# Optimization experiments

Measured on AMD Instinct MI355X. Metric: run time of the kernel, lower is better.

The kernel has to match this reference:

```python
import jax, jax.numpy as jnp
import numpy as np

EPS = 0.07      # sinkhorn temperature
ITERS = 7       # sinkhorn iterations
TINY = 1e-8
NORM_EPS = 1e-12  # F.normalize default clamp


def setup_inputs() -> dict:
    key = jax.random.key(0)
    k1, k2 = jax.random.split(key)
    x = jax.random.normal(k1, (64, 2048, 24, 12), dtype=jnp.float32)
    anchors = jax.random.normal(k2, (2, 2048), dtype=jnp.float32) * 0.02
    return {"x": x, "anchors": anchors}


def reference(x, anchors):
    B, C, H, W = x.shape
    HW = H * W
    # tokens: (B, HW, C)
    X = x.reshape(B, C, HW).transpose(0, 2, 1)
    Xn = X / jnp.maximum(jnp.linalg.norm(X, axis=-1, keepdims=True), NORM_EPS)
    An = anchors / jnp.maximum(jnp.linalg.norm(anchors, axis=-1, keepdims=True), NORM_EPS)
    # cosine cost (B, HW, 2)
    Cmat = 1.0 - jnp.einsum('bhc,kc->bhk', Xn, An)
    Kmat = jnp.exp(-Cmat / max(EPS, TINY)) + TINY
    a = jnp.full((B, HW), 1.0 / HW, dtype=Kmat.dtype)
    b = jnp.full((B, 2), 0.5, dtype=Kmat.dtype)

    def step(carry, _):
        u, v = carry
        Kv = jnp.einsum('bhk,bk->bh', Kmat, v) + TINY
        u = a / Kv
        KTu = jnp.einsum('bhk,bh->bk', Kmat, u) + TINY
        v = b / KTu
        return (u, v), None

    u0 = jnp.ones((B, HW), dtype=Kmat.dtype)
    v0 = jnp.ones((B, 2), dtype=Kmat.dtype)
    (u, v), _ = jax.lax.scan(step, (u0, v0), None, length=ITERS)
    # transport plan and soft masks
    P = Kmat * u[:, :, None] * v[:, None, :]          # (B, HW, 2)
    m = (P * HW).transpose(0, 2, 1).reshape(B, 2, H, W)
    # masked pooling for both prototypes at once
    num = jnp.einsum('bchw,bkhw->bkc', x, m)           # (B, 2, C)
    den = m.sum(axis=(2, 3)) + 1e-6                    # (B, 2)
    c = num / den[:, :, None]
    c0_vec = c[:, 0][:, :, None, None]                 # (B, C, 1, 1)
    c1_vec = c[:, 1][:, :, None, None]
    return (c0_vec, c1_vec, m)
```

## Files before the change

kernel.cpp:

```cpp
#include <hip/hip_runtime.h>

#define B_    64
#define C_    2048
#define HW_   288
#define EPS_  0.07f
#define TINY_ 1e-8f

__device__ __forceinline__ void acc3(const float4 v, float a0, float a1,
                                     float* ssq, float* sd0, float* sd1) {
  ssq[0] += v.x * v.x; ssq[1] += v.y * v.y; ssq[2] += v.z * v.z; ssq[3] += v.w * v.w;
  sd0[0] += v.x * a0;  sd0[1] += v.y * a0;  sd0[2] += v.z * a0;  sd0[3] += v.w * a0;
  sd1[0] += v.x * a1;  sd1[1] += v.y * a1;  sd1[2] += v.z * a1;  sd1[3] += v.w * a1;
}

__global__ __launch_bounds__(256) void k1_partials(
    const float* __restrict__ x, const float* __restrict__ anchors,
    float* __restrict__ part, int nch, int cpc) {
  int bi = blockIdx.x;
  int nblk = nch >> 2;
  int b  = bi / nblk;
  int cg = bi - b * nblk;
  int t = threadIdx.x, lane = t & 63, wid = t >> 6;
  int ch = cg * 4 + wid;
  int c0 = ch * cpc;
  const float* xb = x + ((size_t)b * C_ + c0) * HW_;
  bool tail = lane < 8;

  float ssq[4] = {0,0,0,0}, sd0[4] = {0,0,0,0}, sd1[4] = {0,0,0,0};
  float tsq[4] = {0,0,0,0}, td0[4] = {0,0,0,0}, td1[4] = {0,0,0,0};

#pragma unroll 4
  for (int r = 0; r < cpc; ++r) {
    const float4* xr = (const float4*)(xb + (size_t)r * HW_);
    float a0 = anchors[c0 + r];
    float a1 = anchors[C_ + c0 + r];
    float4 xa = xr[lane];
    acc3(xa, a0, a1, ssq, sd0, sd1);
    if (tail) {
      float4 xc = xr[64 + lane];
      acc3(xc, a0, a1, tsq, td0, td1);
    }
  }

  size_t PS = (size_t)B_ * nch * HW_;
  float* base = part + (size_t)(b * nch + ch) * HW_;
  float4* p0 = (float4*)base;
  float4* p1 = (float4*)(base + PS);
  float4* p2 = (float4*)(base + 2 * PS);
  p0[lane] = make_float4(ssq[0], ssq[1], ssq[2], ssq[3]);
  p1[lane] = make_float4(sd0[0], sd0[1], sd0[2], sd0[3]);
  p2[lane] = make_float4(sd1[0], sd1[1], sd1[2], sd1[3]);
  if (tail) {
    p0[64 + lane] = make_float4(tsq[0], tsq[1], tsq[2], tsq[3]);
    p1[64 + lane] = make_float4(td0[0], td0[1], td0[2], td0[3]);
    p2[64 + lane] = make_float4(td1[0], td1[1], td1[2], td1[3]);
  }
}

__global__ __launch_bounds__(256) void k1b_reduce(
    const float* __restrict__ part, float* __restrict__ red, int nch) {
  int idx = blockIdx.x * 256 + threadIdx.x;
  int plane = idx / (B_ * HW_);
  int rem = idx - plane * (B_ * HW_);
  int b = rem / HW_;
  int h = rem - b * HW_;
  const float* p = part + (size_t)plane * B_ * nch * HW_ + (size_t)b * nch * HW_ + h;
  float s = 0.f;
#pragma unroll 8
  for (int ch = 0; ch < nch; ++ch) s += p[(size_t)ch * HW_];
  red[idx] = s;
}

__device__ __forceinline__ void block_reduce2(
    float& p0, float& p1, volatile float* red0, volatile float* red1,
    int t, int nw) {
  int lane = t & 63, wid = t >> 6;
#pragma unroll
  for (int off = 32; off >= 1; off >>= 1) {
    p0 += __shfl_down(p0, off);
    p1 += __shfl_down(p1, off);
  }
  __syncthreads();
  if (lane == 0) { red0[wid] = p0; red1[wid] = p1; }
  __syncthreads();
  float s0 = 0.f, s1 = 0.f;
  for (int w = 0; w < nw; ++w) { s0 += red0[w]; s1 += red1[w]; }
  p0 = s0; p1 = s1;
}

__global__ __launch_bounds__(320) void k2_sinkhorn(
    const float* __restrict__ red, const float* __restrict__ anchors,
    float* __restrict__ out_m, float* __restrict__ invden) {
  int b = blockIdx.x, t = threadIdx.x;
  __shared__ float red0[8], red1[8];
  const int nw = 5;

  float a0 = 0.f, a1 = 0.f;
  for (int c = t; c < C_; c += 320) {
    float q0 = anchors[c], q1 = anchors[C_ + c];
    a0 += q0 * q0; a1 += q1 * q1;
  }
  block_reduce2(a0, a1, red0, red1, t, nw);
  float ian0 = 1.0f / fmaxf(sqrtf(a0), 1e-12f);
  float ian1 = 1.0f / fmaxf(sqrtf(a1), 1e-12f);

  float K0 = 0.f, K1 = 0.f;
  if (t < HW_) {
    float ssq = red[b * HW_ + t];
    float d0  = red[B_ * HW_ + b * HW_ + t];
    float d1  = red[2 * B_ * HW_ + b * HW_ + t];
    float ixn = 1.0f / fmaxf(sqrtf(ssq), 1e-12f);
    float cos0 = d0 * ixn * ian0;
    float cos1 = d1 * ixn * ian1;
    K0 = expf((cos0 - 1.0f) / EPS_) + TINY_;
    K1 = expf((cos1 - 1.0f) / EPS_) + TINY_;
  }

  float v0 = 1.f, v1 = 1.f, u = 0.f;
  for (int it = 0; it < 7; ++it) {
    if (t < HW_) u = (1.0f / (float)HW_) / (K0 * v0 + K1 * v1 + TINY_);
    float p0 = K0 * u, p1 = K1 * u;
    block_reduce2(p0, p1, red0, red1, t, nw);
    v0 = 0.5f / (p0 + TINY_);
    v1 = 0.5f / (p1 + TINY_);
  }

  float m0 = 0.f, m1 = 0.f;
  if (t < HW_) {
    m0 = K0 * u * v0 * (float)HW_;
    m1 = K1 * u * v1 * (float)HW_;
  }
  float q0 = m0, q1 = m1;
  block_reduce2(q0, q1, red0, red1, t, nw);
  if (t < HW_) {
    out_m[(b * 2 + 0) * HW_ + t] = m0;
    out_m[(b * 2 + 1) * HW_ + t] = m1;
  }
  if (t == 0) {
    invden[b * 2 + 0] = 1.0f / (q0 + 1e-6f);
    invden[b * 2 + 1] = 1.0f / (q1 + 1e-6f);
  }
}

__global__ __launch_bounds__(256) void k3_pool(
    const float* __restrict__ x, const float* __restrict__ m,
    const float* __restrict__ invden, float* __restrict__ out) {
  int bi = blockIdx.x;
  int b = bi >> 3, seg = bi & 7;
  int t = threadIdx.x, oct = t & 7, rl = t >> 3;

  const float4* m0 = (const float4*)(m + (b * 2 + 0) * HW_);
  const float4* m1 = (const float4*)(m + (b * 2 + 1) * HW_);
  float4 w0[9], w1[9];
#pragma unroll
  for (int j = 0; j < 9; ++j) {
    w0[j] = m0[oct * 9 + j];
    w1[j] = m1[oct * 9 + j];
  }
  float inv0 = invden[2 * b], inv1 = invden[2 * b + 1];

  int cbase = seg * 256;
#pragma unroll 2
  for (int g = 0; g < 8; ++g) {
    int c = cbase + g * 32 + rl;
    const float4* xr = (const float4*)(x + ((size_t)b * C_ + c) * HW_) + oct * 9;
    float a0 = 0.f, a1 = 0.f;
#pragma unroll
    for (int j = 0; j < 9; ++j) {
      float4 xa = xr[j];
      a0 += xa.x * w0[j].x + xa.y * w0[j].y + xa.z * w0[j].z + xa.w * w0[j].w;
      a1 += xa.x * w1[j].x + xa.y * w1[j].y + xa.z * w1[j].z + xa.w * w1[j].w;
    }
#pragma unroll
    for (int off = 4; off >= 1; off >>= 1) {
      a0 += __shfl_xor(a0, off);
      a1 += __shfl_xor(a1, off);
    }
    if (oct == 0) {
      out[(size_t)b * C_ + c] = a0 * inv0;
      out[(size_t)B_ * C_ + (size_t)b * C_ + c] = a1 * inv1;
    }
  }
}

extern "C" void kernel_launch(void* const* d_in, const int* in_sizes, int n_in,
                              void* d_out, int out_size, void* d_ws, size_t ws_size,
                              hipStream_t stream) {
  const float* x       = (const float*)d_in[0];
  const float* anchors = (const float*)d_in[1];
  float* out = (float*)d_out;

  float* invden = (float*)d_ws;
  float* red = invden + 128;
  float* part = red + 3 * B_ * HW_;
  int nch = 32;
  while (nch > 4 &&
         (size_t)(128 + 3 * B_ * HW_ + 3 * B_ * nch * HW_) * sizeof(float) > ws_size)
    nch >>= 1;
  int cpc = C_ / nch;

  float* out_m = out + 2 * B_ * C_;

  k1_partials<<<B_ * (nch / 4), 256, 0, stream>>>(x, anchors, part, nch, cpc);
  k1b_reduce<<<(3 * B_ * HW_) / 256, 256, 0, stream>>>(part, red, nch);
  k2_sinkhorn<<<B_, 320, 0, stream>>>(red, anchors, out_m, invden);
  k3_pool<<<B_ * 8, 256, 0, stream>>>(x, out_m, invden, out);
}
```

Measured before the change: 276.5 us.

## Double-buffer k1 loads, spread tail across lanes, double k1/k3 grid parallelism

```diff
diff --git a/kernel.cpp b/kernel.cpp
--- a/kernel.cpp
+++ b/kernel.cpp
@@ -5,6 +5,8 @@
 #define HW_   288
 #define EPS_  0.07f
 #define TINY_ 1e-8f
+#define NCH_  64
+#define CPC_  (C_ / NCH_)
 
 __device__ __forceinline__ void acc3(const float4 v, float a0, float a1,
                                      float* ssq, float* sd0, float* sd1) {
@@ -15,59 +17,83 @@
 
 __global__ __launch_bounds__(256) void k1_partials(
     const float* __restrict__ x, const float* __restrict__ anchors,
-    float* __restrict__ part, int nch, int cpc) {
+    float* __restrict__ part) {
   int bi = blockIdx.x;
-  int nblk = nch >> 2;
-  int b  = bi / nblk;
-  int cg = bi - b * nblk;
+  int b  = bi >> 4;
+  int cg = bi & 15;
   int t = threadIdx.x, lane = t & 63, wid = t >> 6;
   int ch = cg * 4 + wid;
-  int c0 = ch * cpc;
+  int c0 = ch * CPC_;
   const float* xb = x + ((size_t)b * C_ + c0) * HW_;
-  bool tail = lane < 8;
 
   float ssq[4] = {0,0,0,0}, sd0[4] = {0,0,0,0}, sd1[4] = {0,0,0,0};
+
+  float4 buf[4];
+#pragma unroll
+  for (int j = 0; j < 4; ++j)
+    buf[j] = ((const float4*)(xb + (size_t)j * HW_))[lane];
+
+#pragma unroll 1
+  for (int r = 0; r < CPC_; r += 4) {
+    float4 cur[4];
+#pragma unroll
+    for (int j = 0; j < 4; ++j) cur[j] = buf[j];
+    if (r + 4 < CPC_) {
+#pragma unroll
+      for (int j = 0; j < 4; ++j)
+        buf[j] = ((const float4*)(xb + (size_t)(r + 4 + j) * HW_))[lane];
+    }
+#pragma unroll
+    for (int j = 0; j < 4; ++j) {
+      float a0 = anchors[c0 + r + j];
+      float a1 = anchors[C_ + c0 + r + j];
+      acc3(cur[j], a0, a1, ssq, sd0, sd1);
+    }
+  }
+
   float tsq[4] = {0,0,0,0}, td0[4] = {0,0,0,0}, td1[4] = {0,0,0,0};
-
-#pragma unroll 4
-  for (int r = 0; r < cpc; ++r) {
-    const float4* xr = (const float4*)(xb + (size_t)r * HW_);
+  int rg = lane >> 3, q = lane & 7;
+#pragma unroll
+  for (int k = 0; k < CPC_ / 8; ++k) {
+    int r = k * 8 + rg;
+    float4 v = ((const float4*)(xb + (size_t)r * HW_))[64 + q];
     float a0 = anchors[c0 + r];
     float a1 = anchors[C_ + c0 + r];
-    float4 xa = xr[lane];
-    acc3(xa, a0, a1, ssq, sd0, sd1);
-    if (tail) {
-      float4 xc = xr[64 + lane];
-      acc3(xc, a0, a1, tsq, td0, td1);
-    }
-  }
-
-  size_t PS = (size_t)B_ * nch * HW_;
-  float* base = part + (size_t)(b * nch + ch) * HW_;
-  float4* p0 = (float4*)base;
-  float4* p1 = (float4*)(base + PS);
-  float4* p2 = (float4*)(base + 2 * PS);
-  p0[lane] = make_float4(ssq[0], ssq[1], ssq[2], ssq[3]);
-  p1[lane] = make_float4(sd0[0], sd0[1], sd0[2], sd0[3]);
-  p2[lane] = make_float4(sd1[0], sd1[1], sd1[2], sd1[3]);
-  if (tail) {
-    p0[64 + lane] = make_float4(tsq[0], tsq[1], tsq[2], tsq[3]);
-    p1[64 + lane] = make_float4(td0[0], td0[1], td0[2], td0[3]);
-    p2[64 + lane] = make_float4(td1[0], td1[1], td1[2], td1[3]);
+    acc3(v, a0, a1, tsq, td0, td1);
+  }
+#pragma unroll
+  for (int off = 8; off < 64; off <<= 1) {
+#pragma unroll
+    for (int j = 0; j < 4; ++j) {
+      tsq[j] += __shfl_xor(tsq[j], off);
+      td0[j] += __shfl_xor(td0[j], off);
+      td1[j] += __shfl_xor(td1[j], off);
+    }
+  }
+
+  size_t PS = (size_t)B_ * NCH_ * HW_;
+  float* base = part + (size_t)(b * NCH_ + ch) * HW_;
+  ((float4*)base)[lane]          = make_float4(ssq[0], ssq[1], ssq[2], ssq[3]);
+  ((float4*)(base + PS))[lane]   = make_float4(sd0[0], sd0[1], sd0[2], sd0[3]);
+  ((float4*)(base + 2*PS))[lane] = make_float4(sd1[0], sd1[1], sd1[2], sd1[3]);
+  if (lane < 8) {
+    ((float4*)base)[64 + lane]          = make_float4(tsq[0], tsq[1], tsq[2], tsq[3]);
+    ((float4*)(base + PS))[64 + lane]   = make_float4(td0[0], td0[1], td0[2], td0[3]);
+    ((float4*)(base + 2*PS))[64 + lane] = make_float4(td1[0], td1[1], td1[2], td1[3]);
   }
 }
 
 __global__ __launch_bounds__(256) void k1b_reduce(
-    const float* __restrict__ part, float* __restrict__ red, int nch) {
+    const float* __restrict__ part, float* __restrict__ red) {
   int idx = blockIdx.x * 256 + threadIdx.x;
   int plane = idx / (B_ * HW_);
   int rem = idx - plane * (B_ * HW_);
   int b = rem / HW_;
   int h = rem - b * HW_;
-  const float* p = part + (size_t)plane * B_ * nch * HW_ + (size_t)b * nch * HW_ + h;
+  const float* p = part + (size_t)plane * B_ * NCH_ * HW_ + (size_t)b * NCH_ * HW_ + h;
   float s = 0.f;
 #pragma unroll 8
-  for (int ch = 0; ch < nch; ++ch) s += p[(size_t)ch * HW_];
+  for (int ch = 0; ch < NCH_; ++ch) s += p[(size_t)ch * HW_];
   red[idx] = s;
 }
 
@@ -146,7 +172,7 @@
     const float* __restrict__ x, const float* __restrict__ m,
     const float* __restrict__ invden, float* __restrict__ out) {
   int bi = blockIdx.x;
-  int b = bi >> 3, seg = bi & 7;
+  int b = bi >> 4, seg = bi & 15;
   int t = threadIdx.x, oct = t & 7, rl = t >> 3;
 
   const float4* m0 = (const float4*)(m + (b * 2 + 0) * HW_);
@@ -159,17 +185,19 @@
   }
   float inv0 = invden[2 * b], inv1 = invden[2 * b + 1];
 
-  int cbase = seg * 256;
-#pragma unroll 2
-  for (int g = 0; g < 8; ++g) {
+  int cbase = seg * 128;
+#pragma unroll 1
+  for (int g = 0; g < 4; ++g) {
     int c = cbase + g * 32 + rl;
     const float4* xr = (const float4*)(x + ((size_t)b * C_ + c) * HW_) + oct * 9;
+    float4 xa[9];
+#pragma unroll
+    for (int j = 0; j < 9; ++j) xa[j] = xr[j];
     float a0 = 0.f, a1 = 0.f;
 #pragma unroll
     for (int j = 0; j < 9; ++j) {
-      float4 xa = xr[j];
-      a0 += xa.x * w0[j].x + xa.y * w0[j].y + xa.z * w0[j].z + xa.w * w0[j].w;
-      a1 += xa.x * w1[j].x + xa.y * w1[j].y + xa.z * w1[j].z + xa.w * w1[j].w;
+      a0 += xa[j].x * w0[j].x + xa[j].y * w0[j].y + xa[j].z * w0[j].z + xa[j].w * w0[j].w;
+      a1 += xa[j].x * w1[j].x + xa[j].y * w1[j].y + xa[j].z * w1[j].z + xa[j].w * w1[j].w;
     }
 #pragma unroll
     for (int off = 4; off >= 1; off >>= 1) {
@@ -193,16 +221,11 @@
   float* invden = (float*)d_ws;
   float* red = invden + 128;
   float* part = red + 3 * B_ * HW_;
-  int nch = 32;
-  while (nch > 4 &&
-         (size_t)(128 + 3 * B_ * HW_ + 3 * B_ * nch * HW_) * sizeof(float) > ws_size)
-    nch >>= 1;
-  int cpc = C_ / nch;
 
   float* out_m = out + 2 * B_ * C_;
 
-  k1_partials<<<B_ * (nch / 4), 256, 0, stream>>>(x, anchors, part, nch, cpc);
-  k1b_reduce<<<(3 * B_ * HW_) / 256, 256, 0, stream>>>(part, red, nch);
+  k1_partials<<<B_ * (NCH_ / 4), 256, 0, stream>>>(x, anchors, part);
+  k1b_reduce<<<(3 * B_ * HW_) / 256, 256, 0, stream>>>(part, red);
   k2_sinkhorn<<<B_, 320, 0, stream>>>(red, anchors, out_m, invden);
-  k3_pool<<<B_ * 8, 256, 0, stream>>>(x, out_m, invden, out);
-}
+  k3_pool<<<B_ * 16, 256, 0, stream>>>(x, out_m, invden, out);
+}
```

Result: faster. 251.9 us (-8.9%).
